# Optimization experiments

Measured on AMD Instinct MI355X. Metric: run time of the kernel, lower is better.

Reference implementation:

```python
import jax, jax.numpy as jnp
import numpy as np


def _branch(x2d, V, U, v2, v1, u2, u1):
    # x2d: [N, in]; V: [s, in]; U: [out, s]; scales are [1, dim]
    Vq = jnp.sign(V)
    Uq = jnp.sign(U)
    v1u2 = v1 * u2  # [1, s]
    h = (x2d * v2) @ Vq.T          # [N, s]
    y = (h * v1u2) @ Uq.T          # [N, out]
    return y * u1


def setup_inputs() -> dict:
    key = jax.random.key(0)
    ks = jax.random.split(key, 14)
    IN, OUT, S = 4096, 4096, 1024
    B, T = 4, 2048
    f = jax.random.normal
    return {
        "x":    f(ks[0], (B, T, IN), jnp.float32),
        "V":    f(ks[1], (S, IN), jnp.float32),
        "U":    f(ks[2], (OUT, S), jnp.float32),
        "v2":   f(ks[3], (1, IN), jnp.float32),
        "v1":   f(ks[4], (1, S), jnp.float32),
        "u2":   f(ks[5], (1, S), jnp.float32),
        "u1":   f(ks[6], (1, OUT), jnp.float32),
        "V_R":  f(ks[7], (S, IN), jnp.float32),
        "U_R":  f(ks[8], (OUT, S), jnp.float32),
        "v2_R": f(ks[9], (1, IN), jnp.float32),
        "v1_R": f(ks[10], (1, S), jnp.float32),
        "u2_R": f(ks[11], (1, S), jnp.float32),
        "u1_R": f(ks[12], (1, OUT), jnp.float32),
        "bias": f(ks[13], (OUT,), jnp.float32),
    }


def reference(x, V, U, v2, v1, u2, u1, V_R, U_R, v2_R, v1_R, u2_R, u1_R, bias):
    *lead, hidden = x.shape
    x2d = x.reshape(-1, hidden)
    y = _branch(x2d, V, U, v2, v1, u2, u1)
    y = y + _branch(x2d, V_R, U_R, v2_R, v1_R, u2_R, u1_R)
    y = y + bias
    return y.reshape(*lead, bias.shape[0])
```

## Files before the change

### kernel.cpp

```cpp
#include <hip/hip_runtime.h>
#include <hip/hip_bf16.h>
#include <stdint.h>

typedef __bf16 bf16_t;
typedef __attribute__((ext_vector_type(8))) __bf16 bf16x8;
typedef __attribute__((ext_vector_type(4))) float f32x4;

#define DIM_IN  4096
#define DIM_OUT 4096
#define DIM_S   1024
#define DIM_S2  2048
#define NROWS   8192

typedef const __attribute__((address_space(1))) void gvoid_t;
typedef __attribute__((address_space(3))) void lvoid_t;

__device__ __forceinline__ float signf(float v) {
    return (v > 0.f) ? 1.f : ((v < 0.f) ? -1.f : 0.f);
}


__global__ void cast_x_kernel(const float* __restrict__ x, bf16_t* __restrict__ xb) {
    int idx = blockIdx.x * blockDim.x + threadIdx.x;
    const float4* p = reinterpret_cast<const float4*>(x) + (size_t)idx * 2;
    float4 a = p[0], b = p[1];
    bf16x8 o;
    o[0] = (bf16_t)a.x; o[1] = (bf16_t)a.y; o[2] = (bf16_t)a.z; o[3] = (bf16_t)a.w;
    o[4] = (bf16_t)b.x; o[5] = (bf16_t)b.y; o[6] = (bf16_t)b.z; o[7] = (bf16_t)b.w;
    reinterpret_cast<bf16x8*>(xb)[idx] = o;
}

__global__ void build_vcat_kernel(const float* __restrict__ V, const float* __restrict__ v2,
                                  const float* __restrict__ V_R, const float* __restrict__ v2_R,
                                  bf16_t* __restrict__ out) {
    int idx = blockIdx.x * blockDim.x + threadIdx.x;
    int s2 = idx >> 9;
    int i0 = (idx & 511) * 8;
    const float* src; const float* sc;
    if (s2 < DIM_S) { src = V   + (size_t)s2 * DIM_IN;           sc = v2;   }
    else            { src = V_R + (size_t)(s2 - DIM_S) * DIM_IN; sc = v2_R; }
    float4 a  = *reinterpret_cast<const float4*>(src + i0);
    float4 b  = *reinterpret_cast<const float4*>(src + i0 + 4);
    float4 sa = *reinterpret_cast<const float4*>(sc + i0);
    float4 sb = *reinterpret_cast<const float4*>(sc + i0 + 4);
    bf16x8 o;
    o[0] = (bf16_t)(signf(a.x) * sa.x); o[1] = (bf16_t)(signf(a.y) * sa.y);
    o[2] = (bf16_t)(signf(a.z) * sa.z); o[3] = (bf16_t)(signf(a.w) * sa.w);
    o[4] = (bf16_t)(signf(b.x) * sb.x); o[5] = (bf16_t)(signf(b.y) * sb.y);
    o[6] = (bf16_t)(signf(b.z) * sb.z); o[7] = (bf16_t)(signf(b.w) * sb.w);
    reinterpret_cast<bf16x8*>(out)[idx] = o;
}

__global__ void build_wcat_kernel(const float* __restrict__ U, const float* __restrict__ v1,
                                  const float* __restrict__ u2, const float* __restrict__ u1,
                                  const float* __restrict__ U_R, const float* __restrict__ v1_R,
                                  const float* __restrict__ u2_R, const float* __restrict__ u1_R,
                                  bf16_t* __restrict__ out) {
    int idx = blockIdx.x * blockDim.x + threadIdx.x;
    int j  = idx >> 8;
    int s0 = (idx & 255) * 8;
    const float* srcU; const float* sv1; const float* su2; float amp;
    if (s0 < DIM_S) { srcU = U   + (size_t)j * DIM_S + s0; sv1 = v1 + s0;   su2 = u2 + s0;   amp = u1[j];   }
    else { int s = s0 - DIM_S;
           srcU = U_R + (size_t)j * DIM_S + s;  sv1 = v1_R + s; su2 = u2_R + s; amp = u1_R[j]; }
    float4 a  = *reinterpret_cast<const float4*>(srcU);
    float4 b  = *reinterpret_cast<const float4*>(srcU + 4);
    float4 va = *reinterpret_cast<const float4*>(sv1);
    float4 vb = *reinterpret_cast<const float4*>(sv1 + 4);
    float4 ua = *reinterpret_cast<const float4*>(su2);
    float4 ub = *reinterpret_cast<const float4*>(su2 + 4);
    bf16x8 o;
    o[0] = (bf16_t)(amp * va.x * ua.x * signf(a.x));
    o[1] = (bf16_t)(amp * va.y * ua.y * signf(a.y));
    o[2] = (bf16_t)(amp * va.z * ua.z * signf(a.z));
    o[3] = (bf16_t)(amp * va.w * ua.w * signf(a.w));
    o[4] = (bf16_t)(amp * vb.x * ub.x * signf(b.x));
    o[5] = (bf16_t)(amp * vb.y * ub.y * signf(b.y));
    o[6] = (bf16_t)(amp * vb.z * ub.z * signf(b.z));
    o[7] = (bf16_t)(amp * vb.w * ub.w * signf(b.w));
    reinterpret_cast<bf16x8*>(out)[idx] = o;
}


#define VMCNT0() do { asm volatile("s_waitcnt vmcnt(0)" ::: "memory"); \
                      __builtin_amdgcn_sched_barrier(0); } while (0)
#define SB0()    __builtin_amdgcn_sched_barrier(0)

template<int N, int K, bool OUT_BF16>
__global__ __launch_bounds__(512, 2) void gemm256_kernel(
        const bf16_t* __restrict__ A, const bf16_t* __restrict__ B,
        bf16_t* __restrict__ Cb, float* __restrict__ Cf,
        const float* __restrict__ bias) {
    extern __shared__ char lds[];
    constexpr int NT = K / 64;
    static_assert(NT >= 2, "K too small");
    const int tid  = threadIdx.x;
    const int wave = tid >> 6;
    const int lane = tid & 63;
    const int wr = wave >> 2;
    const int wc = wave & 3;

    const int nwg  = gridDim.x;
    const int orig = blockIdx.x;
    const int swz  = (orig & 7) * (nwg >> 3) + (orig >> 3);
    constexpr int NTX = N / 256;
    const int n0 = (swz % NTX) * 256;
    const int m0 = (swz / NTX) * 256;

    char* ldsA = lds;
    char* ldsB = lds + 65536;

    const char* gA[2]; const char* gB[2];
#pragma unroll
    for (int j = 0; j < 2; ++j) {
        int off = j * 8192 + wave * 1024 + lane * 16;
        int lg  = off ^ (((off >> 7) & 7) << 4);
        int row = lg >> 7;
        int cb  = lg & 127;
        gA[j] = (const char*)A + (size_t)(m0 + row) * (K * 2) + cb;
        gB[j] = (const char*)B + (size_t)(n0 + row) * (K * 2) + cb;
    }

#define STAGE_A(t_, mh) do { \
    int _lo = (((t_) & 1) << 15) + ((mh) << 14) + (wave << 10); \
    size_t _ga = (size_t)(mh) * (128 * K * 2) + (size_t)(t_) * 128; \
    __builtin_amdgcn_global_load_lds((gvoid_t*)(gA[0] + _ga), (lvoid_t*)(ldsA + _lo), 16, 0, 0); \
    __builtin_amdgcn_global_load_lds((gvoid_t*)(gA[1] + _ga), (lvoid_t*)(ldsA + _lo + 8192), 16, 0, 0); \
} while (0)
#define STAGE_B(t_, nh) do { \
    int _lo = (((t_) & 1) << 15) + ((nh) << 14) + (wave << 10); \
    size_t _ga = (size_t)(nh) * (128 * K * 2) + (size_t)(t_) * 128; \
    __builtin_amdgcn_global_load_lds((gvoid_t*)(gB[0] + _ga), (lvoid_t*)(ldsB + _lo), 16, 0, 0); \
    __builtin_amdgcn_global_load_lds((gvoid_t*)(gB[1] + _ga), (lvoid_t*)(ldsB + _lo + 8192), 16, 0, 0); \
} while (0)

    const int swzmask = (lane & 7) << 4;
    int abase0, abase1, bbase0, bbase1;
    {
        int araw = (lane & 15) * 128 + ((lane >> 4) << 4);
        abase0 = (araw ^ swzmask) + (wr << 14);
        abase1 = ((araw + 64) ^ swzmask) + (wr << 14);
        int braw = ((wc & 1) * 64 + (lane & 15)) * 128 + ((lane >> 4) << 4);
        bbase0 = (braw ^ swzmask) + ((wc >> 1) << 14);
        bbase1 = ((braw + 64) ^ swzmask) + ((wc >> 1) << 14);
    }

#define RD_A4(dst, base, mg, t_) do { \
    const int _sb = (((t_) & 1) << 15) + (base); \
    _Pragma("unroll") \
    for (int mi = 0; mi < 4; ++mi) \
        dst[mi] = *(const bf16x8*)(ldsA + _sb + ((mg) * 4 + mi) * 2048); \
} while (0)
#define RD_B4(dst, base, t_) do { \
    const int _sb = (((t_) & 1) << 15) + (base); \
    _Pragma("unroll") \
    for (int ni = 0; ni < 4; ++ni) \
        dst[ni] = *(const bf16x8*)(ldsB + _sb + ni * 2048); \
} while (0)
#define MFMA16(mg, AF, BF) do { \
    __builtin_amdgcn_s_setprio(1); \
    _Pragma("unroll") \
    for (int mi = 0; mi < 4; ++mi) \
        _Pragma("unroll") \
        for (int n = 0; n < 4; ++n) \
            acc[(mg) * 4 + mi][n] = __builtin_amdgcn_mfma_f32_16x16x32_bf16( \
                AF[mi], BF[n], acc[(mg) * 4 + mi][n], 0, 0, 0); \
    __builtin_amdgcn_s_setprio(0); \
} while (0)

    f32x4 acc[8][4];
#pragma unroll
    for (int m = 0; m < 8; ++m)
#pragma unroll
        for (int n = 0; n < 4; ++n)
            acc[m][n] = (f32x4){0.f, 0.f, 0.f, 0.f};

    bf16x8 afP[4], afQ[4], bf0[4], bf1[4];

    STAGE_A(0, 0); STAGE_A(0, 1);
    STAGE_B(0, 0); STAGE_B(0, 1);
    VMCNT0();
    __builtin_amdgcn_s_barrier();
    RD_A4(afP, abase0, 0, 0); RD_B4(bf0, bbase0, 0);

    for (int t = 0; t < NT; ++t) {
        const bool i1 = (t + 1 < NT);
        if (i1) { STAGE_A(t + 1, 0); STAGE_A(t + 1, 1); }
        RD_A4(afQ, abase0, 1, t);
        RD_B4(bf1, bbase1, t);
        SB0();
        MFMA16(0, afP, bf0);
        if (i1) { STAGE_B(t + 1, 0); STAGE_B(t + 1, 1); }
        RD_A4(afP, abase1, 0, t);
        SB0();
        MFMA16(1, afQ, bf0);
        RD_A4(afQ, abase1, 1, t);
        SB0();
        MFMA16(0, afP, bf1);
        VMCNT0();
        __builtin_amdgcn_s_barrier();
        if (i1) { RD_A4(afP, abase0, 0, t + 1); RD_B4(bf0, bbase0, t + 1); }
        SB0();
        MFMA16(1, afQ, bf1);
    }

#undef RD_A4
#undef RD_B4
#undef MFMA16
#undef STAGE_A
#undef STAGE_B

    const int cr = (lane >> 4) << 2;
    const int cc = lane & 15;
#pragma unroll
    for (int m = 0; m < 8; ++m) {
        const int row = m0 + wr * 128 + m * 16 + cr;
#pragma unroll
        for (int n = 0; n < 4; ++n) {
            const int col = n0 + wc * 64 + n * 16 + cc;
            if (OUT_BF16) {
#pragma unroll
                for (int j = 0; j < 4; ++j)
                    Cb[(size_t)(row + j) * N + col] = (bf16_t)acc[m][n][j];
            } else {
                const float bv = bias[col];
#pragma unroll
                for (int j = 0; j < 4; ++j)
                    Cf[(size_t)(row + j) * N + col] = acc[m][n][j] + bv;
            }
        }
    }
}

extern "C" void kernel_launch(void* const* d_in, const int* in_sizes, int n_in,
                              void* d_out, int out_size, void* d_ws, size_t ws_size,
                              hipStream_t stream) {
    const float* x    = (const float*)d_in[0];
    const float* V    = (const float*)d_in[1];
    const float* U    = (const float*)d_in[2];
    const float* v2   = (const float*)d_in[3];
    const float* v1   = (const float*)d_in[4];
    const float* u2   = (const float*)d_in[5];
    const float* u1   = (const float*)d_in[6];
    const float* V_R  = (const float*)d_in[7];
    const float* U_R  = (const float*)d_in[8];
    const float* v2_R = (const float*)d_in[9];
    const float* v1_R = (const float*)d_in[10];
    const float* u2_R = (const float*)d_in[11];
    const float* u1_R = (const float*)d_in[12];
    const float* bias = (const float*)d_in[13];
    float* out = (float*)d_out;

    char* ws = (char*)d_ws;
    bf16_t* Xb   = (bf16_t*)(ws);
    bf16_t* Vcat = (bf16_t*)(ws + (size_t)64  * 1024 * 1024);
    bf16_t* Wcat = (bf16_t*)(ws + (size_t)80  * 1024 * 1024);
    bf16_t* Hb   = (bf16_t*)(ws + (size_t)96  * 1024 * 1024);

    (void)hipFuncSetAttribute((const void*)gemm256_kernel<DIM_S2, DIM_IN, true>,
                              hipFuncAttributeMaxDynamicSharedMemorySize, 131072);
    (void)hipFuncSetAttribute((const void*)gemm256_kernel<DIM_OUT, DIM_S2, false>,
                              hipFuncAttributeMaxDynamicSharedMemorySize, 131072);

    cast_x_kernel    <<<16384, 256, 0, stream>>>(x, Xb);
    build_vcat_kernel<<<4096, 256, 0, stream>>>(V, v2, V_R, v2_R, Vcat);
    build_wcat_kernel<<<4096, 256, 0, stream>>>(U, v1, u2, u1, U_R, v1_R, u2_R, u1_R, Wcat);

    gemm256_kernel<DIM_S2, DIM_IN, true>
        <<<(DIM_S2 / 256) * (NROWS / 256), 512, 131072, stream>>>(Xb, Vcat, Hb, nullptr, nullptr);
    gemm256_kernel<DIM_OUT, DIM_S2, false>
        <<<(DIM_OUT / 256) * (NROWS / 256), 512, 131072, stream>>>(Hb, Wcat, nullptr, out, bias);
}
```

Before: 283.6 us.

## Fuse fp32-to-bf16 cast of x into first GEMM's A-tile staging

Removes the separate cast_x kernel and has the first GEMM load fp32 x tiles into registers, convert them to bf16 and write them to LDS, instead of using direct global-to-LDS loads of a precast buffer. This avoids writing and re-reading a 64 MB bf16 copy of x. In exchange, the first GEMM reads twice the A bytes per tile, since x stays fp32 and is re-read by each of the 8 column tiles. It also adds register pressure and extra LDS write and wait instructions to the main loop.

```diff
diff --git a/kernel.cpp b/kernel.cpp
--- a/kernel.cpp
+++ b/kernel.cpp
@@ -19,16 +19,6 @@
     return (v > 0.f) ? 1.f : ((v < 0.f) ? -1.f : 0.f);
 }
 
-
-__global__ void cast_x_kernel(const float* __restrict__ x, bf16_t* __restrict__ xb) {
-    int idx = blockIdx.x * blockDim.x + threadIdx.x;
-    const float4* p = reinterpret_cast<const float4*>(x) + (size_t)idx * 2;
-    float4 a = p[0], b = p[1];
-    bf16x8 o;
-    o[0] = (bf16_t)a.x; o[1] = (bf16_t)a.y; o[2] = (bf16_t)a.z; o[3] = (bf16_t)a.w;
-    o[4] = (bf16_t)b.x; o[5] = (bf16_t)b.y; o[6] = (bf16_t)b.z; o[7] = (bf16_t)b.w;
-    reinterpret_cast<bf16x8*>(xb)[idx] = o;
-}
 
 __global__ void build_vcat_kernel(const float* __restrict__ V, const float* __restrict__ v2,
                                   const float* __restrict__ V_R, const float* __restrict__ v2_R,
@@ -84,11 +74,15 @@
 
 #define VMCNT0() do { asm volatile("s_waitcnt vmcnt(0)" ::: "memory"); \
                       __builtin_amdgcn_sched_barrier(0); } while (0)
+#define VMCNTN(n) do { asm volatile("s_waitcnt vmcnt(" #n ")" ::: "memory"); \
+                      __builtin_amdgcn_sched_barrier(0); } while (0)
+#define LGKM0()  do { asm volatile("s_waitcnt lgkmcnt(0)" ::: "memory"); \
+                      __builtin_amdgcn_sched_barrier(0); } while (0)
 #define SB0()    __builtin_amdgcn_sched_barrier(0)
 
-template<int N, int K, bool OUT_BF16>
+template<int N, int K, bool OUT_BF16, bool A_F32>
 __global__ __launch_bounds__(512, 2) void gemm256_kernel(
-        const bf16_t* __restrict__ A, const bf16_t* __restrict__ B,
+        const void* __restrict__ Aptr, const bf16_t* __restrict__ B,
         bf16_t* __restrict__ Cb, float* __restrict__ Cf,
         const float* __restrict__ bias) {
     extern __shared__ char lds[];
@@ -117,19 +111,46 @@
         int lg  = off ^ (((off >> 7) & 7) << 4);
         int row = lg >> 7;
         int cb  = lg & 127;
-        gA[j] = (const char*)A + (size_t)(m0 + row) * (K * 2) + cb;
+        if (A_F32) gA[j] = (const char*)Aptr + (size_t)(m0 + row) * (K * 4) + cb * 2;
+        else       gA[j] = (const char*)Aptr + (size_t)(m0 + row) * (K * 2) + cb;
         gB[j] = (const char*)B + (size_t)(n0 + row) * (K * 2) + cb;
     }
 
 #define STAGE_A(t_, mh) do { \
     int _lo = (((t_) & 1) << 15) + ((mh) << 14) + (wave << 10); \
-    size_t _ga = (size_t)(mh) * (128 * K * 2) + (size_t)(t_) * 128; \
+    size_t _ga = (size_t)(mh) * (128 * (size_t)K * 2) + (size_t)(t_) * 128; \
     __builtin_amdgcn_global_load_lds((gvoid_t*)(gA[0] + _ga), (lvoid_t*)(ldsA + _lo), 16, 0, 0); \
     __builtin_amdgcn_global_load_lds((gvoid_t*)(gA[1] + _ga), (lvoid_t*)(ldsA + _lo + 8192), 16, 0, 0); \
 } while (0)
+    float4 aL[8];
+#define STAGE_A_LOAD(t_) do { \
+    _Pragma("unroll") \
+    for (int _mh = 0; _mh < 2; ++_mh) \
+        _Pragma("unroll") \
+        for (int _j = 0; _j < 2; ++_j) { \
+            const char* _p = gA[_j] + (size_t)_mh * (128 * (size_t)K * 4) + (size_t)(t_) * 256; \
+            aL[(_mh * 2 + _j) * 2]     = *(const float4*)(_p); \
+            aL[(_mh * 2 + _j) * 2 + 1] = *(const float4*)(_p + 16); \
+        } \
+} while (0)
+#define STAGE_A_WRITE(t_) do { \
+    _Pragma("unroll") \
+    for (int _mh = 0; _mh < 2; ++_mh) \
+        _Pragma("unroll") \
+        for (int _j = 0; _j < 2; ++_j) { \
+            int _lo = (((t_) & 1) << 15) + (_mh << 14) + (wave << 10) + _j * 8192 + lane * 16; \
+            float4 _r0 = aL[(_mh * 2 + _j) * 2], _r1 = aL[(_mh * 2 + _j) * 2 + 1]; \
+            bf16x8 _w; \
+            _w[0] = (bf16_t)_r0.x; _w[1] = (bf16_t)_r0.y; \
+            _w[2] = (bf16_t)_r0.z; _w[3] = (bf16_t)_r0.w; \
+            _w[4] = (bf16_t)_r1.x; _w[5] = (bf16_t)_r1.y; \
+            _w[6] = (bf16_t)_r1.z; _w[7] = (bf16_t)_r1.w; \
+            *(bf16x8*)(ldsA + _lo) = _w; \
+        } \
+} while (0)
 #define STAGE_B(t_, nh) do { \
     int _lo = (((t_) & 1) << 15) + ((nh) << 14) + (wave << 10); \
-    size_t _ga = (size_t)(nh) * (128 * K * 2) + (size_t)(t_) * 128; \
+    size_t _ga = (size_t)(nh) * (128 * (size_t)K * 2) + (size_t)(t_) * 128; \
     __builtin_amdgcn_global_load_lds((gvoid_t*)(gB[0] + _ga), (lvoid_t*)(ldsB + _lo), 16, 0, 0); \
     __builtin_amdgcn_global_load_lds((gvoid_t*)(gB[1] + _ga), (lvoid_t*)(ldsB + _lo + 8192), 16, 0, 0); \
 } while (0)
@@ -177,15 +198,27 @@
 
     bf16x8 afP[4], afQ[4], bf0[4], bf1[4];
 
-    STAGE_A(0, 0); STAGE_A(0, 1);
-    STAGE_B(0, 0); STAGE_B(0, 1);
-    VMCNT0();
+    if (A_F32) {
+        STAGE_A_LOAD(0);
+        STAGE_B(0, 0); STAGE_B(0, 1);
+        VMCNTN(4);
+        STAGE_A_WRITE(0);
+        VMCNT0();
+        LGKM0();
+    } else {
+        STAGE_A(0, 0); STAGE_A(0, 1);
+        STAGE_B(0, 0); STAGE_B(0, 1);
+        VMCNT0();
+    }
     __builtin_amdgcn_s_barrier();
     RD_A4(afP, abase0, 0, 0); RD_B4(bf0, bbase0, 0);
 
     for (int t = 0; t < NT; ++t) {
         const bool i1 = (t + 1 < NT);
-        if (i1) { STAGE_A(t + 1, 0); STAGE_A(t + 1, 1); }
+        if (i1) {
+            if (A_F32) STAGE_A_LOAD(t + 1);
+            else { STAGE_A(t + 1, 0); STAGE_A(t + 1, 1); }
+        }
         RD_A4(afQ, abase0, 1, t);
         RD_B4(bf1, bbase1, t);
         SB0();
@@ -195,9 +228,11 @@
         SB0();
         MFMA16(1, afQ, bf0);
         RD_A4(afQ, abase1, 1, t);
+        if (A_F32) { if (i1) { VMCNTN(4); STAGE_A_WRITE(t + 1); } }
         SB0();
         MFMA16(0, afP, bf1);
         VMCNT0();
+        if (A_F32) LGKM0();
         __builtin_amdgcn_s_barrier();
         if (i1) { RD_A4(afP, abase0, 0, t + 1); RD_B4(bf0, bbase0, t + 1); }
         SB0();
@@ -208,6 +243,8 @@
 #undef RD_B4
 #undef MFMA16
 #undef STAGE_A
+#undef STAGE_A_LOAD
+#undef STAGE_A_WRITE
 #undef STAGE_B
 
     const int cr = (lane >> 4) << 2;
@@ -252,22 +289,20 @@
     float* out = (float*)d_out;
 
     char* ws = (char*)d_ws;
-    bf16_t* Xb   = (bf16_t*)(ws);
-    bf16_t* Vcat = (bf16_t*)(ws + (size_t)64  * 1024 * 1024);
-    bf16_t* Wcat = (bf16_t*)(ws + (size_t)80  * 1024 * 1024);
-    bf16_t* Hb   = (bf16_t*)(ws + (size_t)96  * 1024 * 1024);
-
-    (void)hipFuncSetAttribute((const void*)gemm256_kernel<DIM_S2, DIM_IN, true>,
+    bf16_t* Vcat = (bf16_t*)(ws);
+    bf16_t* Wcat = (bf16_t*)(ws + (size_t)16 * 1024 * 1024);
+    bf16_t* Hb   = (bf16_t*)(ws + (size_t)32 * 1024 * 1024);
+
+    (void)hipFuncSetAttribute((const void*)gemm256_kernel<DIM_S2, DIM_IN, true, true>,
                               hipFuncAttributeMaxDynamicSharedMemorySize, 131072);
-    (void)hipFuncSetAttribute((const void*)gemm256_kernel<DIM_OUT, DIM_S2, false>,
+    (void)hipFuncSetAttribute((const void*)gemm256_kernel<DIM_OUT, DIM_S2, false, false>,
                               hipFuncAttributeMaxDynamicSharedMemorySize, 131072);
 
-    cast_x_kernel    <<<16384, 256, 0, stream>>>(x, Xb);
     build_vcat_kernel<<<4096, 256, 0, stream>>>(V, v2, V_R, v2_R, Vcat);
     build_wcat_kernel<<<4096, 256, 0, stream>>>(U, v1, u2, u1, U_R, v1_R, u2_R, u1_R, Wcat);
 
-    gemm256_kernel<DIM_S2, DIM_IN, true>
-        <<<(DIM_S2 / 256) * (NROWS / 256), 512, 131072, stream>>>(Xb, Vcat, Hb, nullptr, nullptr);
-    gemm256_kernel<DIM_OUT, DIM_S2, false>
+    gemm256_kernel<DIM_S2, DIM_IN, true, true>
+        <<<(DIM_S2 / 256) * (NROWS / 256), 512, 131072, stream>>>(x, Vcat, Hb, nullptr, nullptr);
+    gemm256_kernel<DIM_OUT, DIM_S2, false, false>
         <<<(DIM_OUT / 256) * (NROWS / 256), 512, 131072, stream>>>(Hb, Wcat, nullptr, out, bias);
 }
```

New measurement: 337.5 us. 1.19x slower.
